# Performance work log

Hardware: AMD Instinct MI355X
Metric: run time of the kernel (lower is better)

The kernel has to match this reference:

```python
import jax, jax.numpy as jnp
import numpy as np

B, S, D = 128, 512, 512  # source requires S == hidden_dim for bmm(Q^T, K^T) to type-check


def setup_inputs() -> dict:
    key = jax.random.key(0)
    ks = jax.random.split(key, 7)
    scale = 1.0 / np.sqrt(D)
    return {
        "x": jax.random.normal(ks[0], (B, S, D), dtype=jnp.float32),
        "Wq": jax.random.uniform(ks[1], (D, D), jnp.float32, -scale, scale),
        "bq": jax.random.uniform(ks[2], (D,), jnp.float32, -scale, scale),
        "Wk": jax.random.uniform(ks[3], (D, D), jnp.float32, -scale, scale),
        "bk": jax.random.uniform(ks[4], (D,), jnp.float32, -scale, scale),
        "Wv": jax.random.uniform(ks[5], (D, D), jnp.float32, -scale, scale),
        "bv": jax.random.uniform(ks[6], (D,), jnp.float32, -scale, scale),
    }


def reference(x, Wq, bq, Wk, bk, Wv, bv):
    # nn.Linear: y = x @ W^T + b
    Q = jnp.einsum("bsd,ed->bse", x, Wq) + bq  # (B,S,D)
    K = jnp.einsum("bsd,ed->bse", x, Wk) + bk
    V = jnp.einsum("bsd,ed->bse", x, Wv) + bv
    Qp = jnp.transpose(Q, (0, 2, 1))  # (B,D,S)
    Kp = jnp.transpose(K, (0, 2, 1))  # (B,D,S); bmm needs S == D
    energy = jnp.matmul(Qp, Kp)       # (B,D,D) -- unscaled, as in source
    attention = jax.nn.softmax(energy, axis=2)
    Vp = jnp.transpose(V, (0, 2, 1))  # (B,D,S)
    context = jnp.matmul(attention, Vp)  # (B,D,S)
    return jnp.transpose(context, (0, 2, 1))  # (B,S,D)
```

## Files before the change

### kernel.cpp

```cpp
#include <hip/hip_runtime.h>
#include <hip/hip_bf16.h>


#define NDIM 512
#define NBATCH 128
constexpr size_t SD = (size_t)NDIM * NDIM;

typedef __attribute__((ext_vector_type(8))) short bf16x8;
typedef __attribute__((ext_vector_type(4))) float f32x4;

typedef const __attribute__((address_space(1))) unsigned int* gas_ptr;
typedef __attribute__((address_space(3))) unsigned int* las_ptr;

struct alignas(8) us4 { unsigned short x, y, z, w; };
struct alignas(4) us2 { unsigned short x, y; };

__device__ __forceinline__ void gl_lds16(const void* g, void* lds) {
    __builtin_amdgcn_global_load_lds((gas_ptr)g, (las_ptr)lds, 16, 0, 0);
}
__device__ __forceinline__ unsigned short f2bf(float x) {
    return __builtin_bit_cast(unsigned short, __float2bfloat16(x));
}
__device__ __forceinline__ float bf2f(unsigned short u) {
    return __bfloat162float(__builtin_bit_cast(__hip_bfloat16, u));
}

template<int NSEG, int EPI, int BIAS>
__global__ __launch_bounds__(512, 2) void gemm8_nt(
    const unsigned short* a0, const unsigned short* a1, const unsigned short* a2, long sA,
    const unsigned short* b0, const unsigned short* b1, const unsigned short* b2, long sB,
    void* c0v, void* c1v, long sC, const float* __restrict__ bias)
{
    constexpr int NTK = NSEG * 8;
    __shared__ unsigned short AS[2][256 * 64];
    __shared__ unsigned short BS[2][256 * 64];

    const int nwg = gridDim.x;
    int id = blockIdx.x;
    int wg = ((nwg & 7) == 0) ? ((id & 7) * (nwg >> 3) + (id >> 3)) : id;
    const int z  = wg >> 2;
    const int m0 = ((wg >> 1) & 1) * 256;
    const int n0 = (wg & 1) * 256;

    const int tid = threadIdx.x;
    const int l = tid & 63, w = tid >> 6;
    const int wr = w >> 2, wc = w & 3;

    const size_t zA = (size_t)z * sA + (size_t)m0 * NDIM;
    const size_t zB = (size_t)z * sB + (size_t)n0 * NDIM;

    const int srow = tid >> 3;
    const int scol = (((tid & 7) ^ ((tid >> 3) & 7)) << 3);
    const int ldst = tid * 8;

    auto segA = [&](int s) {
        const unsigned short* p = a0;
        if constexpr (NSEG > 1) { if (s == 1) p = a1; else if (s == 2) p = a2; }
        return p;
    };
    auto segB = [&](int s) {
        const unsigned short* p = b0;
        if constexpr (NSEG > 1) { if (s == 1) p = b1; else if (s == 2) p = b2; }
        return p;
    };
    auto stageA = [&](int kt, int H, int slot) {
        const int seg = kt >> 3, k0 = (kt & 7) << 6;
        const unsigned short* g = segA(seg) + zA;
        #pragma unroll
        for (int j = 0; j < 2; ++j)
            gl_lds16(g + (size_t)(H * 128 + j * 64 + srow) * NDIM + k0 + scol,
                     &AS[slot][H * 8192 + j * 4096 + ldst]);
    };
    auto stageB = [&](int kt, int H, int slot) {
        const int seg = kt >> 3, k0 = (kt & 7) << 6;
        const unsigned short* g = segB(seg) + zB;
        #pragma unroll
        for (int j = 0; j < 2; ++j)
            gl_lds16(g + (size_t)(H * 128 + j * 64 + srow) * NDIM + k0 + scol,
                     &BS[slot][H * 8192 + j * 4096 + ldst]);
    };

    auto readA = [&](int slot, int H, bf16x8 (&dst)[4][2]) {
        #pragma unroll
        for (int mi = 0; mi < 4; ++mi) {
            const int row = H * 128 + wr * 64 + mi * 16 + (l & 15);
            #pragma unroll
            for (int kk = 0; kk < 2; ++kk) {
                const int s16 = ((kk << 2) + (l >> 4)) ^ (l & 7);
                dst[mi][kk] = *(const bf16x8*)&AS[slot][row * 64 + s16 * 8];
            }
        }
    };
    auto readB = [&](int slot, int H, bf16x8 (&dst)[2][2]) {
        #pragma unroll
        for (int ni = 0; ni < 2; ++ni) {
            const int row = H * 128 + wc * 32 + ni * 16 + (l & 15);
            #pragma unroll
            for (int kk = 0; kk < 2; ++kk) {
                const int s16 = ((kk << 2) + (l >> 4)) ^ (l & 7);
                dst[ni][kk] = *(const bf16x8*)&BS[slot][row * 64 + s16 * 8];
            }
        }
    };
    auto mfma16 = [&](f32x4 (&ac)[4][2], const bf16x8 (&a)[4][2],
                      const bf16x8 (&b)[2][2]) {
        __builtin_amdgcn_s_setprio(1);
        #pragma unroll
        for (int mi = 0; mi < 4; ++mi)
            #pragma unroll
            for (int ni = 0; ni < 2; ++ni)
                #pragma unroll
                for (int kk = 0; kk < 2; ++kk)
                    ac[mi][ni] = __builtin_amdgcn_mfma_f32_16x16x32_bf16(
                        a[mi][kk], b[ni][kk], ac[mi][ni], 0, 0, 0);
        __builtin_amdgcn_s_setprio(0);
    };

    f32x4 acc[2][2][4][2] = {};

    stageA(0, 0, 0); stageB(0, 0, 0); stageB(0, 1, 0); stageA(0, 1, 0);
    asm volatile("s_waitcnt vmcnt(4)" ::: "memory");
    asm volatile("s_barrier" ::: "memory");

    for (int kt = 0; kt < NTK; ++kt) {
        const int cur = kt & 1, nxt = cur ^ 1;
        const int ktn = (kt + 1 < NTK) ? kt + 1 : kt;
        bf16x8 a0f[4][2], a1f[4][2], b0f[2][2], b1f[2][2];

        readA(cur, 0, a0f); readB(cur, 0, b0f);
        stageA(ktn, 0, nxt); stageB(ktn, 0, nxt);
        asm volatile("s_waitcnt vmcnt(6)" ::: "memory");
        asm volatile("s_barrier" ::: "memory");
        asm volatile("s_waitcnt lgkmcnt(0)" ::: "memory");
        __builtin_amdgcn_sched_barrier(0);
        mfma16(acc[0][0], a0f, b0f);

        readB(cur, 1, b1f);
        stageB(ktn, 1, nxt);
        asm volatile("s_waitcnt vmcnt(6)" ::: "memory");
        asm volatile("s_barrier" ::: "memory");
        asm volatile("s_waitcnt lgkmcnt(0)" ::: "memory");
        __builtin_amdgcn_sched_barrier(0);
        mfma16(acc[0][1], a0f, b1f);

        readA(cur, 1, a1f);
        stageA(ktn, 1, nxt);
        asm volatile("s_waitcnt vmcnt(8)" ::: "memory");
        asm volatile("s_barrier" ::: "memory");
        asm volatile("s_waitcnt lgkmcnt(0)" ::: "memory");
        __builtin_amdgcn_sched_barrier(0);
        mfma16(acc[1][1], a1f, b1f);

        asm volatile("s_waitcnt vmcnt(4)" ::: "memory");
        asm volatile("s_barrier" ::: "memory");
        __builtin_amdgcn_sched_barrier(0);
        mfma16(acc[1][0], a1f, b0f);
    }
    asm volatile("s_waitcnt vmcnt(0) lgkmcnt(0)" ::: "memory");

    const size_t zc = (size_t)z * sC;
    const int cr = (l >> 4) << 2;
    const int cc = l & 15;
    #pragma unroll
    for (int Qr = 0; Qr < 2; ++Qr) {
        #pragma unroll
        for (int Qc = 0; Qc < 2; ++Qc) {
            #pragma unroll
            for (int mi = 0; mi < 4; ++mi) {
                #pragma unroll
                for (int r = 0; r < 4; ++r) {
                    const int m = m0 + Qr * 128 + wr * 64 + mi * 16 + cr + r;
                    const float bm = (BIAS == 1) ? bias[m] : 0.0f;
                    #pragma unroll
                    for (int ni = 0; ni < 2; ++ni) {
                        const int n = n0 + Qc * 128 + wc * 32 + ni * 16 + cc;
                        float v = acc[Qr][Qc][mi][ni][r] + bm + ((BIAS == 2) ? bias[n] : 0.0f);
                        const size_t idx = zc + (size_t)m * NDIM + n;
                        if (EPI == 0) {
                            ((float*)c0v)[idx] = v;
                        } else if (EPI == 1) {
                            ((unsigned short*)c0v)[idx] = f2bf(v);
                        } else {
                            const unsigned short h = f2bf(v);
                            ((unsigned short*)c0v)[idx] = h;
                            ((unsigned short*)c1v)[idx] = f2bf(v - bf2f(h));
                        }
                    }
                }
            }
        }
    }
}

template<int NSEG, int EPI, int BIAS>
__global__ __launch_bounds__(256) void gemm_bf16_nt(
    const unsigned short* a0, const unsigned short* a1, const unsigned short* a2, long sA,
    const unsigned short* b0, const unsigned short* b1, const unsigned short* b2, long sB,
    void* c0v, void* c1v, long sC, const float* __restrict__ bias)
{
    __shared__ unsigned short As[128 * 64];
    __shared__ unsigned short Bs[128 * 64];

    const int z  = blockIdx.z;
    const int m0 = blockIdx.y * 128, n0 = blockIdx.x * 128;
    const int tid = threadIdx.x;
    const int l = tid & 63, w = tid >> 6;
    const int wr = w >> 1, wc = w & 1;

    const int srow = tid >> 3;
    const int scol = (tid & 7) << 3;
    unsigned short* ldsA = &As[tid * 8];
    unsigned short* ldsB = &Bs[tid * 8];

    f32x4 acc[4][4] = {};

    const unsigned short* Asegs[3] = {a0, a1, a2};
    const unsigned short* Bsegs[3] = {b0, b1, b2};

    #pragma unroll
    for (int s = 0; s < NSEG; ++s) {
        const unsigned short* Ab = Asegs[s] + (size_t)z * sA + (size_t)m0 * NDIM;
        const unsigned short* Bb = Bsegs[s] + (size_t)z * sB + (size_t)n0 * NDIM;
        for (int k0 = 0; k0 < NDIM; k0 += 64) {
            __syncthreads();
            #pragma unroll
            for (int i = 0; i < 4; ++i) {
                gl_lds16(Ab + (size_t)(srow + i * 32) * NDIM + k0 + scol, ldsA + i * 2048);
                gl_lds16(Bb + (size_t)(srow + i * 32) * NDIM + k0 + scol, ldsB + i * 2048);
            }
            __syncthreads();
            #pragma unroll
            for (int kk = 0; kk < 2; ++kk) {
                bf16x8 af[4], bfv[4];
                #pragma unroll
                for (int f = 0; f < 4; ++f) {
                    af[f]  = *(const bf16x8*)&As[(wr * 64 + f * 16 + (l & 15)) * 64 + kk * 32 + (l >> 4) * 8];
                    bfv[f] = *(const bf16x8*)&Bs[(wc * 64 + f * 16 + (l & 15)) * 64 + kk * 32 + (l >> 4) * 8];
                }
                #pragma unroll
                for (int mi = 0; mi < 4; ++mi)
                    #pragma unroll
                    for (int ni = 0; ni < 4; ++ni)
                        acc[mi][ni] = __builtin_amdgcn_mfma_f32_16x16x32_bf16(
                            af[mi], bfv[ni], acc[mi][ni], 0, 0, 0);
            }
        }
    }

    const size_t zc = (size_t)z * sC;
    const int cr = (l >> 4) << 2;
    const int cc = l & 15;
    #pragma unroll
    for (int mi = 0; mi < 4; ++mi) {
        #pragma unroll
        for (int r = 0; r < 4; ++r) {
            const int m = m0 + wr * 64 + mi * 16 + cr + r;
            const float bm = (BIAS == 1) ? bias[m] : 0.0f;
            #pragma unroll
            for (int ni = 0; ni < 4; ++ni) {
                const int n = n0 + wc * 64 + ni * 16 + cc;
                float v = acc[mi][ni][r] + bm + ((BIAS == 2) ? bias[n] : 0.0f);
                const size_t idx = zc + (size_t)m * NDIM + n;
                if (EPI == 0) {
                    ((float*)c0v)[idx] = v;
                } else if (EPI == 1) {
                    ((unsigned short*)c0v)[idx] = f2bf(v);
                } else {
                    const unsigned short h = f2bf(v);
                    ((unsigned short*)c0v)[idx] = h;
                    ((unsigned short*)c1v)[idx] = f2bf(v - bf2f(h));
                }
            }
        }
    }
}

__global__ __launch_bounds__(256) void softmax_bf16(
    const float* __restrict__ E, unsigned short* __restrict__ A)
{
    const int l  = threadIdx.x & 63;
    const int wv = threadIdx.x >> 6;
    const size_t row = (size_t)blockIdx.x * 4 + wv;
    const float* p = E + row * NDIM;
    unsigned short* q = A + row * NDIM;

    const float4 v0 = ((const float4*)p)[l * 2];
    const float4 v1 = ((const float4*)p)[l * 2 + 1];

    float mx = fmaxf(fmaxf(fmaxf(v0.x, v0.y), fmaxf(v0.z, v0.w)),
                     fmaxf(fmaxf(v1.x, v1.y), fmaxf(v1.z, v1.w)));
    #pragma unroll
    for (int s = 32; s > 0; s >>= 1) mx = fmaxf(mx, __shfl_xor(mx, s, 64));

    float e0 = __expf(v0.x - mx), e1 = __expf(v0.y - mx);
    float e2 = __expf(v0.z - mx), e3 = __expf(v0.w - mx);
    float e4 = __expf(v1.x - mx), e5 = __expf(v1.y - mx);
    float e6 = __expf(v1.z - mx), e7 = __expf(v1.w - mx);
    float sm = ((e0 + e1) + (e2 + e3)) + ((e4 + e5) + (e6 + e7));
    #pragma unroll
    for (int s = 32; s > 0; s >>= 1) sm += __shfl_xor(sm, s, 64);

    const float inv = 1.0f / sm;
    us4 o0, o1;
    o0.x = f2bf(e0 * inv); o0.y = f2bf(e1 * inv);
    o0.z = f2bf(e2 * inv); o0.w = f2bf(e3 * inv);
    o1.x = f2bf(e4 * inv); o1.y = f2bf(e5 * inv);
    o1.z = f2bf(e6 * inv); o1.w = f2bf(e7 * inv);
    ((us4*)q)[l * 2]     = o0;
    ((us4*)q)[l * 2 + 1] = o1;
}

template<bool LO>
__global__ __launch_bounds__(256) void split_to_bf16(
    const float* __restrict__ src,
    unsigned short* __restrict__ hi, unsigned short* __restrict__ lo, int n4)
{
    const int i = blockIdx.x * 256 + threadIdx.x;
    if (i >= n4) return;
    const float4 v = ((const float4*)src)[i];
    us4 h;
    h.x = f2bf(v.x); h.y = f2bf(v.y); h.z = f2bf(v.z); h.w = f2bf(v.w);
    ((us4*)hi)[i] = h;
    if (LO) {
        us4 g;
        g.x = f2bf(v.x - bf2f(h.x)); g.y = f2bf(v.y - bf2f(h.y));
        g.z = f2bf(v.z - bf2f(h.z)); g.w = f2bf(v.w - bf2f(h.w));
        ((us4*)lo)[i] = g;
    }
}

extern "C" void kernel_launch(void* const* d_in, const int* in_sizes, int n_in,
                              void* d_out, int out_size, void* d_ws, size_t ws_size,
                              hipStream_t stream)
{
    const float* x  = (const float*)d_in[0];
    const float* Wq = (const float*)d_in[1];
    const float* bq = (const float*)d_in[2];
    const float* Wk = (const float*)d_in[3];
    const float* bk = (const float*)d_in[4];
    const float* Wv = (const float*)d_in[5];
    const float* bv = (const float*)d_in[6];
    float* out = (float*)d_out;

    long units = (long)(ws_size / (2 * SD));
    long cl = (units - 6) / 10;
    if (cl < 1) cl = 1;
    int c = 1;
    while (c * 2 <= cl && c < 128) c *= 2;
    const bool use8 = (c >= 64);
    if (!use8 && c > 32) c = 32;

    unsigned short* p = (unsigned short*)d_ws;
    auto take = [&](size_t elems) { unsigned short* r = p; p += elems; return r; };
    unsigned short* WqH = take(SD);
    unsigned short* WqL = take(SD);
    unsigned short* WkH = take(SD);
    unsigned short* WkL = take(SD);
    unsigned short* WvH = take(SD);
    unsigned short* xH  = take((size_t)c * SD);
    unsigned short* xL  = take((size_t)c * SD);
    unsigned short* QH  = take((size_t)c * SD);
    unsigned short* QL  = take((size_t)c * SD);
    unsigned short* KH  = take((size_t)c * SD);
    unsigned short* KL  = take((size_t)c * SD);
    unsigned short* Vb  = take((size_t)c * SD);
    unsigned short* Ab  = take((size_t)c * SD);
    float* Ew = (float*)p;

    const int n4w = (int)(SD / 4);
    split_to_bf16<true ><<<dim3((n4w + 255) / 256), dim3(256), 0, stream>>>(Wq, WqH, WqL, n4w);
    split_to_bf16<true ><<<dim3((n4w + 255) / 256), dim3(256), 0, stream>>>(Wk, WkH, WkL, n4w);
    split_to_bf16<false><<<dim3((n4w + 255) / 256), dim3(256), 0, stream>>>(Wv, WvH, nullptr, n4w);

    for (int b0 = 0; b0 < NBATCH; b0 += c) {
        const int cb = (NBATCH - b0 < c) ? (NBATCH - b0) : c;
        const int n4 = (int)((size_t)cb * SD / 4);
        split_to_bf16<true><<<dim3((n4 + 255) / 256), dim3(256), 0, stream>>>(
            x + (size_t)b0 * SD, xH, xL, n4);

        if (use8) {
            const dim3 g(4 * cb), blk(512);
            gemm8_nt<3, 2, 1><<<g, blk, 0, stream>>>(
                WqH, WqL, WqH, 0,  xH, xH, xL, (long)SD,  QH, QL, (long)SD, bq);
            gemm8_nt<3, 2, 2><<<g, blk, 0, stream>>>(
                xH, xL, xH, (long)SD,  WkH, WkH, WkL, 0,  KH, KL, (long)SD, bk);
            gemm8_nt<1, 1, 2><<<g, blk, 0, stream>>>(
                xH, nullptr, nullptr, (long)SD,  WvH, nullptr, nullptr, 0,  Vb, nullptr, (long)SD, bv);
            gemm8_nt<3, 0, 0><<<g, blk, 0, stream>>>(
                QH, QL, QH, (long)SD,  KH, KH, KL, (long)SD,  Ew, nullptr, (long)SD, nullptr);
            softmax_bf16<<<dim3(cb * NDIM / 4), dim3(256), 0, stream>>>(Ew, Ab);
            gemm8_nt<1, 0, 0><<<g, blk, 0, stream>>>(
                Vb, nullptr, nullptr, (long)SD,  Ab, nullptr, nullptr, (long)SD,
                out + (size_t)b0 * SD, nullptr, (long)SD, nullptr);
        } else {
            const dim3 g(4, 4, cb), blk(256);
            gemm_bf16_nt<3, 2, 1><<<g, blk, 0, stream>>>(
                WqH, WqL, WqH, 0,  xH, xH, xL, (long)SD,  QH, QL, (long)SD, bq);
            gemm_bf16_nt<3, 2, 2><<<g, blk, 0, stream>>>(
                xH, xL, xH, (long)SD,  WkH, WkH, WkL, 0,  KH, KL, (long)SD, bk);
            gemm_bf16_nt<1, 1, 2><<<g, blk, 0, stream>>>(
                xH, nullptr, nullptr, (long)SD,  WvH, nullptr, nullptr, 0,  Vb, nullptr, (long)SD, bv);
            gemm_bf16_nt<3, 0, 0><<<g, blk, 0, stream>>>(
                QH, QL, QH, (long)SD,  KH, KH, KL, (long)SD,  Ew, nullptr, (long)SD, nullptr);
            softmax_bf16<<<dim3(cb * NDIM / 4), dim3(256), 0, stream>>>(Ew, Ab);
            gemm_bf16_nt<1, 0, 0><<<g, blk, 0, stream>>>(
                Vb, nullptr, nullptr, (long)SD,  Ab, nullptr, nullptr, (long)SD,
                out + (size_t)b0 * SD, nullptr, (long)SD, nullptr);
        }
    }
}
```

Measured before the change: 545.8 us.

## Fuse split-bf16 three-term GEMMs into one K-loop sharing hi/lo tile loads

Adds a gemm8_fused3 kernel for the split-precision GEMMs (AH*BH + AL*BH + AH*BL). Instead of walking the concatenated K three times, it stages the four hi/lo panels per 32-wide K step and reuses the loaded AH and BH fragments across two MFMA passes. Global traffic drops from six panel-loads to four per K step. It also reshapes the tile into 32-wide K panels with a new swizzle and rewrites the barrier/wait schedule. The generic gemm8_nt's last two MFMA groups are merged under a single wait, which also trims a barrier.

```diff
diff --git a/kernel.cpp b/kernel.cpp
--- a/kernel.cpp
+++ b/kernel.cpp
@@ -25,15 +25,17 @@
     return __bfloat162float(__builtin_bit_cast(__hip_bfloat16, u));
 }
 
-template<int NSEG, int EPI, int BIAS>
-__global__ __launch_bounds__(512, 2) void gemm8_nt(
-    const unsigned short* a0, const unsigned short* a1, const unsigned short* a2, long sA,
-    const unsigned short* b0, const unsigned short* b1, const unsigned short* b2, long sB,
+template<int EPI, int BIAS>
+__global__ __launch_bounds__(512, 2) void gemm8_fused3(
+    const unsigned short* aH, const unsigned short* aL, long sA,
+    const unsigned short* bH, const unsigned short* bL, long sB,
     void* c0v, void* c1v, long sC, const float* __restrict__ bias)
 {
-    constexpr int NTK = NSEG * 8;
-    __shared__ unsigned short AS[2][256 * 64];
-    __shared__ unsigned short BS[2][256 * 64];
+    constexpr int NTK = 16;
+    __shared__ unsigned short AHs[2][8192];
+    __shared__ unsigned short ALs[2][8192];
+    __shared__ unsigned short BHs[2][8192];
+    __shared__ unsigned short BLs[2][8192];
 
     const int nwg = gridDim.x;
     int id = blockIdx.x;
@@ -46,115 +48,92 @@
     const int l = tid & 63, w = tid >> 6;
     const int wr = w >> 2, wc = w & 3;
 
-    const size_t zA = (size_t)z * sA + (size_t)m0 * NDIM;
-    const size_t zB = (size_t)z * sB + (size_t)n0 * NDIM;
-
-    const int srow = tid >> 3;
-    const int scol = (((tid & 7) ^ ((tid >> 3) & 7)) << 3);
-    const int ldst = tid * 8;
-
-    auto segA = [&](int s) {
-        const unsigned short* p = a0;
-        if constexpr (NSEG > 1) { if (s == 1) p = a1; else if (s == 2) p = a2; }
-        return p;
-    };
-    auto segB = [&](int s) {
-        const unsigned short* p = b0;
-        if constexpr (NSEG > 1) { if (s == 1) p = b1; else if (s == 2) p = b2; }
-        return p;
-    };
-    auto stageA = [&](int kt, int H, int slot) {
-        const int seg = kt >> 3, k0 = (kt & 7) << 6;
-        const unsigned short* g = segA(seg) + zA;
-        #pragma unroll
-        for (int j = 0; j < 2; ++j)
-            gl_lds16(g + (size_t)(H * 128 + j * 64 + srow) * NDIM + k0 + scol,
-                     &AS[slot][H * 8192 + j * 4096 + ldst]);
-    };
-    auto stageB = [&](int kt, int H, int slot) {
-        const int seg = kt >> 3, k0 = (kt & 7) << 6;
-        const unsigned short* g = segB(seg) + zB;
-        #pragma unroll
-        for (int j = 0; j < 2; ++j)
-            gl_lds16(g + (size_t)(H * 128 + j * 64 + srow) * NDIM + k0 + scol,
-                     &BS[slot][H * 8192 + j * 4096 + ldst]);
-    };
-
-    auto readA = [&](int slot, int H, bf16x8 (&dst)[4][2]) {
-        #pragma unroll
-        for (int mi = 0; mi < 4; ++mi) {
-            const int row = H * 128 + wr * 64 + mi * 16 + (l & 15);
-            #pragma unroll
-            for (int kk = 0; kk < 2; ++kk) {
-                const int s16 = ((kk << 2) + (l >> 4)) ^ (l & 7);
-                dst[mi][kk] = *(const bf16x8*)&AS[slot][row * 64 + s16 * 8];
-            }
-        }
-    };
-    auto readB = [&](int slot, int H, bf16x8 (&dst)[2][2]) {
-        #pragma unroll
-        for (int ni = 0; ni < 2; ++ni) {
-            const int row = H * 128 + wc * 32 + ni * 16 + (l & 15);
-            #pragma unroll
-            for (int kk = 0; kk < 2; ++kk) {
-                const int s16 = ((kk << 2) + (l >> 4)) ^ (l & 7);
-                dst[ni][kk] = *(const bf16x8*)&BS[slot][row * 64 + s16 * 8];
-            }
-        }
-    };
-    auto mfma16 = [&](f32x4 (&ac)[4][2], const bf16x8 (&a)[4][2],
-                      const bf16x8 (&b)[2][2]) {
+    const unsigned short* gAH = aH + (size_t)z * sA + (size_t)m0 * NDIM;
+    const unsigned short* gAL = aL + (size_t)z * sA + (size_t)m0 * NDIM;
+    const unsigned short* gBH = bH + (size_t)z * sB + (size_t)n0 * NDIM;
+    const unsigned short* gBL = bL + (size_t)z * sB + (size_t)n0 * NDIM;
+
+    auto stage = [&](const unsigned short* g, unsigned short* panel, int kt) {
+        const int k0 = kt << 5;
+        #pragma unroll
+        for (int s = 0; s < 2; ++s) {
+            const int G = s * 512 + tid;
+            const int r = G >> 2, gp = G & 3;
+            gl_lds16(g + (size_t)r * NDIM + k0 + ((gp ^ ((r >> 1) & 3)) << 3),
+                     panel + G * 8);
+        }
+    };
+    auto readA = [&](const unsigned short* panel, bf16x8 (&dst)[2][4]) {
+        #pragma unroll
+        for (int H = 0; H < 2; ++H)
+            #pragma unroll
+            for (int mi = 0; mi < 4; ++mi) {
+                const int row = H * 128 + wr * 64 + mi * 16 + (l & 15);
+                const int gp = (l >> 4) ^ ((row >> 1) & 3);
+                dst[H][mi] = *(const bf16x8*)&panel[row * 32 + gp * 8];
+            }
+    };
+    auto readB = [&](const unsigned short* panel, bf16x8 (&dst)[2][2]) {
+        #pragma unroll
+        for (int H = 0; H < 2; ++H)
+            #pragma unroll
+            for (int ni = 0; ni < 2; ++ni) {
+                const int row = H * 128 + wc * 32 + ni * 16 + (l & 15);
+                const int gp = (l >> 4) ^ ((row >> 1) & 3);
+                dst[H][ni] = *(const bf16x8*)&panel[row * 32 + gp * 8];
+            }
+    };
+
+    f32x4 acc[2][2][4][2] = {};
+
+    auto mfma32 = [&](const bf16x8 (&a)[2][4], const bf16x8 (&b)[2][2]) {
         __builtin_amdgcn_s_setprio(1);
         #pragma unroll
-        for (int mi = 0; mi < 4; ++mi)
-            #pragma unroll
-            for (int ni = 0; ni < 2; ++ni)
+        for (int Qr = 0; Qr < 2; ++Qr)
+            #pragma unroll
+            for (int Qc = 0; Qc < 2; ++Qc)
                 #pragma unroll
-                for (int kk = 0; kk < 2; ++kk)
-                    ac[mi][ni] = __builtin_amdgcn_mfma_f32_16x16x32_bf16(
-                        a[mi][kk], b[ni][kk], ac[mi][ni], 0, 0, 0);
+                for (int mi = 0; mi < 4; ++mi)
+                    #pragma unroll
+                    for (int ni = 0; ni < 2; ++ni)
+                        acc[Qr][Qc][mi][ni] = __builtin_amdgcn_mfma_f32_16x16x32_bf16(
+                            a[Qr][mi], b[Qc][ni], acc[Qr][Qc][mi][ni], 0, 0, 0);
         __builtin_amdgcn_s_setprio(0);
     };
 
-    f32x4 acc[2][2][4][2] = {};
-
-    stageA(0, 0, 0); stageB(0, 0, 0); stageB(0, 1, 0); stageA(0, 1, 0);
+    stage(gAH, AHs[0], 0); stage(gBH, BHs[0], 0);
+    stage(gAL, ALs[0], 0); stage(gBL, BLs[0], 0);
     asm volatile("s_waitcnt vmcnt(4)" ::: "memory");
     asm volatile("s_barrier" ::: "memory");
 
     for (int kt = 0; kt < NTK; ++kt) {
         const int cur = kt & 1, nxt = cur ^ 1;
         const int ktn = (kt + 1 < NTK) ? kt + 1 : kt;
-        bf16x8 a0f[4][2], a1f[4][2], b0f[2][2], b1f[2][2];
-
-        readA(cur, 0, a0f); readB(cur, 0, b0f);
-        stageA(ktn, 0, nxt); stageB(ktn, 0, nxt);
+        bf16x8 ah[2][4], al[2][4], bh[2][2], bl[2][2];
+
+        readA(AHs[cur], ah); readB(BHs[cur], bh);
+        stage(gAH, AHs[nxt], ktn); stage(gBH, BHs[nxt], ktn);
         asm volatile("s_waitcnt vmcnt(6)" ::: "memory");
         asm volatile("s_barrier" ::: "memory");
         asm volatile("s_waitcnt lgkmcnt(0)" ::: "memory");
         __builtin_amdgcn_sched_barrier(0);
-        mfma16(acc[0][0], a0f, b0f);
-
-        readB(cur, 1, b1f);
-        stageB(ktn, 1, nxt);
+        mfma32(ah, bh);
+
+        readA(ALs[cur], al);
+        stage(gAL, ALs[nxt], ktn);
         asm volatile("s_waitcnt vmcnt(6)" ::: "memory");
         asm volatile("s_barrier" ::: "memory");
         asm volatile("s_waitcnt lgkmcnt(0)" ::: "memory");
         __builtin_amdgcn_sched_barrier(0);
-        mfma16(acc[0][1], a0f, b1f);
-
-        readA(cur, 1, a1f);
-        stageA(ktn, 1, nxt);
-        asm volatile("s_waitcnt vmcnt(8)" ::: "memory");
+        mfma32(al, bh);
+
+        readB(BLs[cur], bl);
+        stage(gBL, BLs[nxt], ktn);
+        asm volatile("s_waitcnt vmcnt(4)" ::: "memory");
         asm volatile("s_barrier" ::: "memory");
         asm volatile("s_waitcnt lgkmcnt(0)" ::: "memory");
         __builtin_amdgcn_sched_barrier(0);
-        mfma16(acc[1][1], a1f, b1f);
-
-        asm volatile("s_waitcnt vmcnt(4)" ::: "memory");
-        asm volatile("s_barrier" ::: "memory");
-        __builtin_amdgcn_sched_barrier(0);
-        mfma16(acc[1][0], a1f, b0f);
+        mfma32(ah, bl);
     }
     asm volatile("s_waitcnt vmcnt(0) lgkmcnt(0)" ::: "memory");
 
@@ -193,6 +172,171 @@
 }
 
 template<int NSEG, int EPI, int BIAS>
+__global__ __launch_bounds__(512, 2) void gemm8_nt(
+    const unsigned short* a0, const unsigned short* a1, const unsigned short* a2, long sA,
+    const unsigned short* b0, const unsigned short* b1, const unsigned short* b2, long sB,
+    void* c0v, void* c1v, long sC, const float* __restrict__ bias)
+{
+    constexpr int NTK = NSEG * 8;
+    __shared__ unsigned short AS[2][256 * 64];
+    __shared__ unsigned short BS[2][256 * 64];
+
+    const int nwg = gridDim.x;
+    int id = blockIdx.x;
+    int wg = ((nwg & 7) == 0) ? ((id & 7) * (nwg >> 3) + (id >> 3)) : id;
+    const int z  = wg >> 2;
+    const int m0 = ((wg >> 1) & 1) * 256;
+    const int n0 = (wg & 1) * 256;
+
+    const int tid = threadIdx.x;
+    const int l = tid & 63, w = tid >> 6;
+    const int wr = w >> 2, wc = w & 3;
+
+    const size_t zA = (size_t)z * sA + (size_t)m0 * NDIM;
+    const size_t zB = (size_t)z * sB + (size_t)n0 * NDIM;
+
+    const int srow = tid >> 3;
+    const int scol = (((tid & 7) ^ ((tid >> 3) & 7)) << 3);
+    const int ldst = tid * 8;
+
+    auto segA = [&](int s) {
+        const unsigned short* p = a0;
+        if constexpr (NSEG > 1) { if (s == 1) p = a1; }
+        if constexpr (NSEG > 2) { if (s == 2) p = a2; }
+        return p;
+    };
+    auto segB = [&](int s) {
+        const unsigned short* p = b0;
+        if constexpr (NSEG > 1) { if (s == 1) p = b1; }
+        if constexpr (NSEG > 2) { if (s == 2) p = b2; }
+        return p;
+    };
+    auto stageA = [&](int kt, int H, int slot) {
+        const int seg = kt >> 3, k0 = (kt & 7) << 6;
+        const unsigned short* g = segA(seg) + zA;
+        #pragma unroll
+        for (int j = 0; j < 2; ++j)
+            gl_lds16(g + (size_t)(H * 128 + j * 64 + srow) * NDIM + k0 + scol,
+                     &AS[slot][H * 8192 + j * 4096 + ldst]);
+    };
+    auto stageB = [&](int kt, int H, int slot) {
+        const int seg = kt >> 3, k0 = (kt & 7) << 6;
+        const unsigned short* g = segB(seg) + zB;
+        #pragma unroll
+        for (int j = 0; j < 2; ++j)
+            gl_lds16(g + (size_t)(H * 128 + j * 64 + srow) * NDIM + k0 + scol,
+                     &BS[slot][H * 8192 + j * 4096 + ldst]);
+    };
+
+    auto readA = [&](int slot, int H, bf16x8 (&dst)[4][2]) {
+        #pragma unroll
+        for (int mi = 0; mi < 4; ++mi) {
+            const int row = H * 128 + wr * 64 + mi * 16 + (l & 15);
+            #pragma unroll
+            for (int kk = 0; kk < 2; ++kk) {
+                const int s16 = ((kk << 2) + (l >> 4)) ^ (l & 7);
+                dst[mi][kk] = *(const bf16x8*)&AS[slot][row * 64 + s16 * 8];
+            }
+        }
+    };
+    auto readB = [&](int slot, int H, bf16x8 (&dst)[2][2]) {
+        #pragma unroll
+        for (int ni = 0; ni < 2; ++ni) {
+            const int row = H * 128 + wc * 32 + ni * 16 + (l & 15);
+            #pragma unroll
+            for (int kk = 0; kk < 2; ++kk) {
+                const int s16 = ((kk << 2) + (l >> 4)) ^ (l & 7);
+                dst[ni][kk] = *(const bf16x8*)&BS[slot][row * 64 + s16 * 8];
+            }
+        }
+    };
+    auto mfma16 = [&](f32x4 (&ac)[4][2], const bf16x8 (&a)[4][2],
+                      const bf16x8 (&b)[2][2]) {
+        __builtin_amdgcn_s_setprio(1);
+        #pragma unroll
+        for (int mi = 0; mi < 4; ++mi)
+            #pragma unroll
+            for (int ni = 0; ni < 2; ++ni)
+                #pragma unroll
+                for (int kk = 0; kk < 2; ++kk)
+                    ac[mi][ni] = __builtin_amdgcn_mfma_f32_16x16x32_bf16(
+                        a[mi][kk], b[ni][kk], ac[mi][ni], 0, 0, 0);
+        __builtin_amdgcn_s_setprio(0);
+    };
+
+    f32x4 acc[2][2][4][2] = {};
+
+    stageA(0, 0, 0); stageB(0, 0, 0); stageB(0, 1, 0); stageA(0, 1, 0);
+    asm volatile("s_waitcnt vmcnt(4)" ::: "memory");
+    asm volatile("s_barrier" ::: "memory");
+
+    for (int kt = 0; kt < NTK; ++kt) {
+        const int cur = kt & 1, nxt = cur ^ 1;
+        const int ktn = (kt + 1 < NTK) ? kt + 1 : kt;
+        bf16x8 a0f[4][2], a1f[4][2], b0f[2][2], b1f[2][2];
+
+        readA(cur, 0, a0f); readB(cur, 0, b0f);
+        stageA(ktn, 0, nxt); stageB(ktn, 0, nxt);
+        asm volatile("s_waitcnt vmcnt(6)" ::: "memory");
+        asm volatile("s_barrier" ::: "memory");
+        asm volatile("s_waitcnt lgkmcnt(0)" ::: "memory");
+        __builtin_amdgcn_sched_barrier(0);
+        mfma16(acc[0][0], a0f, b0f);
+
+        readB(cur, 1, b1f);
+        stageB(ktn, 1, nxt);
+        asm volatile("s_waitcnt vmcnt(6)" ::: "memory");
+        asm volatile("s_barrier" ::: "memory");
+        asm volatile("s_waitcnt lgkmcnt(0)" ::: "memory");
+        __builtin_amdgcn_sched_barrier(0);
+        mfma16(acc[0][1], a0f, b1f);
+
+        readA(cur, 1, a1f);
+        stageA(ktn, 1, nxt);
+        asm volatile("s_waitcnt vmcnt(4)" ::: "memory");
+        asm volatile("s_barrier" ::: "memory");
+        asm volatile("s_waitcnt lgkmcnt(0)" ::: "memory");
+        __builtin_amdgcn_sched_barrier(0);
+        mfma16(acc[1][1], a1f, b1f);
+        mfma16(acc[1][0], a1f, b0f);
+    }
+    asm volatile("s_waitcnt vmcnt(0) lgkmcnt(0)" ::: "memory");
+
+    const size_t zc = (size_t)z * sC;
+    const int cr = (l >> 4) << 2;
+    const int cc = l & 15;
+    #pragma unroll
+    for (int Qr = 0; Qr < 2; ++Qr) {
+        #pragma unroll
+        for (int Qc = 0; Qc < 2; ++Qc) {
+            #pragma unroll
+            for (int mi = 0; mi < 4; ++mi) {
+                #pragma unroll
+                for (int r = 0; r < 4; ++r) {
+                    const int m = m0 + Qr * 128 + wr * 64 + mi * 16 + cr + r;
+                    const float bm = (BIAS == 1) ? bias[m] : 0.0f;
+                    #pragma unroll
+                    for (int ni = 0; ni < 2; ++ni) {
+                        const int n = n0 + Qc * 128 + wc * 32 + ni * 16 + cc;
+                        float v = acc[Qr][Qc][mi][ni][r] + bm + ((BIAS == 2) ? bias[n] : 0.0f);
+                        const size_t idx = zc + (size_t)m * NDIM + n;
+                        if (EPI == 0) {
+                            ((float*)c0v)[idx] = v;
+                        } else if (EPI == 1) {
+                            ((unsigned short*)c0v)[idx] = f2bf(v);
+                        } else {
+                            const unsigned short h = f2bf(v);
+                            ((unsigned short*)c0v)[idx] = h;
+                            ((unsigned short*)c1v)[idx] = f2bf(v - bf2f(h));
+                        }
+                    }
+                }
+            }
+        }
+    }
+}
+
+template<int NSEG, int EPI, int BIAS>
 __global__ __launch_bounds__(256) void gemm_bf16_nt(
     const unsigned short* a0, const unsigned short* a1, const unsigned short* a2, long sA,
     const unsigned short* b0, const unsigned short* b1, const unsigned short* b2, long sB,
@@ -380,14 +524,14 @@
 
         if (use8) {
             const dim3 g(4 * cb), blk(512);
-            gemm8_nt<3, 2, 1><<<g, blk, 0, stream>>>(
-                WqH, WqL, WqH, 0,  xH, xH, xL, (long)SD,  QH, QL, (long)SD, bq);
-            gemm8_nt<3, 2, 2><<<g, blk, 0, stream>>>(
-                xH, xL, xH, (long)SD,  WkH, WkH, WkL, 0,  KH, KL, (long)SD, bk);
+            gemm8_fused3<2, 1><<<g, blk, 0, stream>>>(
+                WqH, WqL, 0,  xH, xL, (long)SD,  QH, QL, (long)SD, bq);
+            gemm8_fused3<2, 2><<<g, blk, 0, stream>>>(
+                xH, xL, (long)SD,  WkH, WkL, 0,  KH, KL, (long)SD, bk);
             gemm8_nt<1, 1, 2><<<g, blk, 0, stream>>>(
                 xH, nullptr, nullptr, (long)SD,  WvH, nullptr, nullptr, 0,  Vb, nullptr, (long)SD, bv);
-            gemm8_nt<3, 0, 0><<<g, blk, 0, stream>>>(
-                QH, QL, QH, (long)SD,  KH, KH, KL, (long)SD,  Ew, nullptr, (long)SD, nullptr);
+            gemm8_fused3<0, 0><<<g, blk, 0, stream>>>(
+                QH, QL, (long)SD,  KH, KL, (long)SD,  Ew, nullptr, (long)SD, nullptr);
             softmax_bf16<<<dim3(cb * NDIM / 4), dim3(256), 0, stream>>>(Ew, Ab);
             gemm8_nt<1, 0, 0><<<g, blk, 0, stream>>>(
                 Vb, nullptr, nullptr, (long)SD,  Ab, nullptr, nullptr, (long)SD,
```

After: 520.8 us. 4.6% less time.
